# Kernel optimization log

Measured on AMD Instinct MI355X. Metric: run time of the kernel, lower is better.

Reference implementation:

```python
import jax, jax.numpy as jnp
import numpy as np

N = 100000      # nodes
E = 1600000     # edges (avg degree 16)
F_IN = 128
F_OUT = 128
EPS = 1e-5      # BatchNorm eps


def setup_inputs() -> dict:
    key = jax.random.key(0)
    ks = jax.random.split(key, 10)
    s_in = 1.0 / np.sqrt(F_IN)
    s_out = 1.0 / np.sqrt(F_OUT)
    return {
        "x": jax.random.normal(ks[0], (N, F_IN), dtype=jnp.float32),
        "edge_index": jax.random.randint(ks[1], (2, E), 0, N, dtype=jnp.int32),
        # layer 0: SAGEConv(F_IN, F_OUT, aggr='max'); lin_l has bias, lin_r does not
        "W0_l": jax.random.normal(ks[2], (F_IN, F_OUT), dtype=jnp.float32) * s_in,
        "b0_l": jnp.zeros((F_OUT,), dtype=jnp.float32),
        "W0_r": jax.random.normal(ks[3], (F_IN, F_OUT), dtype=jnp.float32) * s_in,
        "gamma0": jnp.ones((F_OUT,), dtype=jnp.float32),
        "beta0": jnp.zeros((F_OUT,), dtype=jnp.float32),
        # layer 1: SAGEConv(F_OUT, F_OUT, aggr='max')
        "W1_l": jax.random.normal(ks[4], (F_OUT, F_OUT), dtype=jnp.float32) * s_out,
        "b1_l": jnp.zeros((F_OUT,), dtype=jnp.float32),
        "W1_r": jax.random.normal(ks[5], (F_OUT, F_OUT), dtype=jnp.float32) * s_out,
        "gamma1": jnp.ones((F_OUT,), dtype=jnp.float32),
        "beta1": jnp.zeros((F_OUT,), dtype=jnp.float32),
    }


def _sage_conv_max(x, src, dst, W_l, b_l, W_r):
    # gather source features along edges, scatter-max into destination nodes
    msgs = x[src]                                             # [E, F]
    agg = jax.ops.segment_max(msgs, dst, num_segments=N)      # [N, F], -inf for isolated
    agg = jnp.where(jnp.isfinite(agg), agg, 0.0)              # PyG fills empty segments with 0
    return agg @ W_l + b_l + x @ W_r                          # lin_l(aggr) + lin_r(x)


def _batch_norm(h, gamma, beta):
    mu = jnp.mean(h, axis=0)
    var = jnp.var(h, axis=0)
    return (h - mu) * jax.lax.rsqrt(var + EPS) * gamma + beta


def reference(x, edge_index, W0_l, b0_l, W0_r, gamma0, beta0,
              W1_l, b1_l, W1_r, gamma1, beta1):
    src, dst = edge_index[0], edge_index[1]
    h = _sage_conv_max(x, src, dst, W0_l, b0_l, W0_r)
    h = jax.nn.relu(_batch_norm(h, gamma0, beta0))
    h = _sage_conv_max(h, src, dst, W1_l, b1_l, W1_r)
    h = jax.nn.relu(_batch_norm(h, gamma1, beta1))
    return h
```

## Files before the change

kernel.cpp:

```cpp
#include <hip/hip_runtime.h>
#include <stdint.h>

#define EPS_BN 1e-5f

typedef __attribute__((ext_vector_type(8))) short short8v;
typedef __attribute__((ext_vector_type(4))) float f32x4;

__device__ __forceinline__ unsigned rne_bf16(float f) {
    unsigned u = __float_as_uint(f);
    return (u + 0x7FFFu + ((u >> 16) & 1u)) >> 16;
}

extern "C" __global__ __launch_bounds__(256)
void f32_to_bf16_kernel(const float4* __restrict__ in, uint2* __restrict__ out, long n4) {
    long i = (long)blockIdx.x * 256 + threadIdx.x;
    long stride = (long)gridDim.x * 256;
    for (; i < n4; i += stride) {
        float4 v = in[i];
        uint2 o;
        o.x = rne_bf16(v.x) | (rne_bf16(v.y) << 16);
        o.y = rne_bf16(v.z) | (rne_bf16(v.w) << 16);
        out[i] = o;
    }
}

extern "C" __global__ __launch_bounds__(256)
void wt_prep_kernel(const float* __restrict__ Wl, const float* __restrict__ Wr,
                    unsigned short* __restrict__ Wt) {
    int idx = blockIdx.x * 256 + threadIdx.x;
    int col = idx >> 8, k = idx & 255;
    float v = (k < 128) ? Wl[(size_t)k * 128 + col] : Wr[(size_t)(k - 128) * 128 + col];
    Wt[(size_t)col * 256 + k] = (unsigned short)rne_bf16(v);
}

extern "C" __global__ __launch_bounds__(256)
void init_head_kernel(int* __restrict__ head, int n) {
    int i = blockIdx.x * 256 + threadIdx.x;
    if (i < n) head[i] = -1;
}

extern "C" __global__ __launch_bounds__(256)
void link_kernel(const int* __restrict__ ei, int* __restrict__ head,
                 uint2* __restrict__ pair, int E) {
    int e = blockIdx.x * 256 + threadIdx.x;
    if (e < E) {
        int src = ei[e];
        int dst = ei[E + e];
        int old = atomicExch(&head[dst], e);
        uint2 p; p.x = (unsigned)src; p.y = (unsigned)old;
        pair[e] = p;
    }
}

extern "C" __global__ __launch_bounds__(256, 8)
void gather_max_ll16_kernel(const uint4* __restrict__ x16r, const int* __restrict__ head,
                            const uint2* __restrict__ pair,
                            uint4* __restrict__ agg16, float* __restrict__ stats, int Nn) {
    if (blockIdx.x == 0 && threadIdx.x < 256) stats[threadIdx.x] = 0.0f;
    int t = blockIdx.x * 256 + threadIdx.x;
    int node = t >> 4;
    if (node >= Nn) return;
    int lane = t & 15;
    int e = head[node];
    uint4 out;
    if (e >= 0) {
        uint2 p = pair[e];
        uint4 r = x16r[(size_t)p.x * 16 + lane];
        float a0 = __uint_as_float(r.x << 16), a1 = __uint_as_float(r.x);
        float a2 = __uint_as_float(r.y << 16), a3 = __uint_as_float(r.y);
        float a4 = __uint_as_float(r.z << 16), a5 = __uint_as_float(r.z);
        float a6 = __uint_as_float(r.w << 16), a7 = __uint_as_float(r.w);
        int en = (int)p.y;
        while (en >= 0) {
            uint2 pn = pair[en];
            uint4 v = x16r[(size_t)pn.x * 16 + lane];
            en = (int)pn.y;
            a0 = fmaxf(a0, __uint_as_float(v.x << 16));
            a1 = fmaxf(a1, __uint_as_float(v.x));
            a2 = fmaxf(a2, __uint_as_float(v.y << 16));
            a3 = fmaxf(a3, __uint_as_float(v.y));
            a4 = fmaxf(a4, __uint_as_float(v.z << 16));
            a5 = fmaxf(a5, __uint_as_float(v.z));
            a6 = fmaxf(a6, __uint_as_float(v.w << 16));
            a7 = fmaxf(a7, __uint_as_float(v.w));
        }
        out.x = (__float_as_uint(a0) >> 16) | (__float_as_uint(a1) & 0xFFFF0000u);
        out.y = (__float_as_uint(a2) >> 16) | (__float_as_uint(a3) & 0xFFFF0000u);
        out.z = (__float_as_uint(a4) >> 16) | (__float_as_uint(a5) & 0xFFFF0000u);
        out.w = (__float_as_uint(a6) >> 16) | (__float_as_uint(a7) & 0xFFFF0000u);
    } else {
        out.x = out.y = out.z = out.w = 0u;
    }
    agg16[(size_t)node * 16 + lane] = out;
}

extern "C" __global__ __launch_bounds__(256)
void gemm_bf16_kernel(const unsigned short* __restrict__ agg16,
                      const unsigned short* __restrict__ xin16,
                      const unsigned short* __restrict__ Wt,
                      const float* __restrict__ bias,
                      float* __restrict__ h, float* __restrict__ stats, int nrows) {
    __shared__ float redS[4][128];
    __shared__ float redQ[4][128];

    const int t = threadIdx.x;
    const int w = t >> 6, l = t & 63;
    const int wm = w >> 1, wn = w & 1;
    const int r16 = l & 15, g = l >> 4;
    const int blockRow = blockIdx.x * 128;
    const int colBase = wn * 64;

    f32x4 acc[4][4];
#pragma unroll
    for (int m = 0; m < 4; ++m)
#pragma unroll
        for (int n = 0; n < 4; ++n) acc[m][n] = (f32x4){0.f, 0.f, 0.f, 0.f};

    const short8v az = {0, 0, 0, 0, 0, 0, 0, 0};

#pragma unroll
    for (int kt = 0; kt < 8; ++kt) {
        const unsigned short* Asrc = (kt < 4) ? agg16 : xin16;
        const int kofs = (kt < 4) ? kt * 32 : kt * 32 - 128;

        short8v b[4];
#pragma unroll
        for (int n = 0; n < 4; ++n) {
            int col = colBase + n * 16 + r16;
            b[n] = *(const short8v*)(Wt + (size_t)col * 256 + kt * 32 + g * 8);
        }
        short8v a[4];
#pragma unroll
        for (int m = 0; m < 4; ++m) {
            int row = blockRow + wm * 64 + m * 16 + r16;
            a[m] = (row < nrows)
                 ? *(const short8v*)(Asrc + (size_t)row * 128 + kofs + g * 8)
                 : az;
        }
#pragma unroll
        for (int m = 0; m < 4; ++m)
#pragma unroll
            for (int n = 0; n < 4; ++n)
                acc[m][n] = __builtin_amdgcn_mfma_f32_16x16x32_bf16(a[m], b[n], acc[m][n], 0, 0, 0);
    }

    for (int i = t; i < 512; i += 256) {
        ((float*)redS)[i] = 0.f;
        ((float*)redQ)[i] = 0.f;
    }
    __syncthreads();

    float bcol[4];
#pragma unroll
    for (int n = 0; n < 4; ++n) bcol[n] = bias[colBase + n * 16 + r16];

    float s4[4] = {0.f, 0.f, 0.f, 0.f};
    float q4[4] = {0.f, 0.f, 0.f, 0.f};
#pragma unroll
    for (int m = 0; m < 4; ++m) {
#pragma unroll
        for (int reg = 0; reg < 4; ++reg) {
            int row = blockRow + wm * 64 + m * 16 + g * 4 + reg;
            if (row < nrows) {
#pragma unroll
                for (int n = 0; n < 4; ++n) {
                    float o = acc[m][n][reg] + bcol[n];
                    h[(size_t)row * 128 + colBase + n * 16 + r16] = o;
                    s4[n] += o;
                    q4[n] += o * o;
                }
            }
        }
    }
#pragma unroll
    for (int n = 0; n < 4; ++n) {
        s4[n] += __shfl_xor(s4[n], 16, 64);
        s4[n] += __shfl_xor(s4[n], 32, 64);
        q4[n] += __shfl_xor(q4[n], 16, 64);
        q4[n] += __shfl_xor(q4[n], 32, 64);
    }
    if (g == 0) {
#pragma unroll
        for (int n = 0; n < 4; ++n) {
            redS[w][colBase + n * 16 + r16] = s4[n];
            redQ[w][colBase + n * 16 + r16] = q4[n];
        }
    }
    __syncthreads();
    if (t < 128) {
        float s = redS[0][t] + redS[1][t] + redS[2][t] + redS[3][t];
        float q = redQ[0][t] + redQ[1][t] + redQ[2][t] + redQ[3][t];
        atomicAdd(&stats[t], s);
        atomicAdd(&stats[128 + t], q);
    }
}

extern "C" __global__
void zero_stats_kernel(float* __restrict__ stats) {
    stats[threadIdx.x] = 0.0f;
}

extern "C" __global__
void finalize_kernel(const float* __restrict__ stats, const float* __restrict__ gamma,
                     const float* __restrict__ beta, float* __restrict__ ss, float inv_n) {
    int c = threadIdx.x;
    if (c < 128) {
        float mu = stats[c] * inv_n;
        float var = stats[128 + c] * inv_n - mu * mu;
        float sc = gamma[c] * rsqrtf(var + EPS_BN);
        ss[c] = sc;
        ss[128 + c] = beta[c] - mu * sc;
    }
}

extern "C" __global__ __launch_bounds__(256)
void bn_relu_tobf16_kernel(const float4* __restrict__ h, const float* __restrict__ ss,
                           uint2* __restrict__ y16, long n4) {
    __shared__ float s_ss[256];
    if (threadIdx.x < 256) s_ss[threadIdx.x] = ss[threadIdx.x];
    __syncthreads();
    long i = (long)blockIdx.x * blockDim.x + threadIdx.x;
    long stride = (long)gridDim.x * blockDim.x;
    for (; i < n4; i += stride) {
        int c4 = (int)(i & 31) * 4;
        float4 v = h[i];
        float o0 = fmaxf(fmaf(v.x, s_ss[c4 + 0], s_ss[128 + c4 + 0]), 0.f);
        float o1 = fmaxf(fmaf(v.y, s_ss[c4 + 1], s_ss[128 + c4 + 1]), 0.f);
        float o2 = fmaxf(fmaf(v.z, s_ss[c4 + 2], s_ss[128 + c4 + 2]), 0.f);
        float o3 = fmaxf(fmaf(v.w, s_ss[c4 + 3], s_ss[128 + c4 + 3]), 0.f);
        uint2 o;
        o.x = rne_bf16(o0) | (rne_bf16(o1) << 16);
        o.y = rne_bf16(o2) | (rne_bf16(o3) << 16);
        y16[i] = o;
    }
}

extern "C" __global__ __launch_bounds__(256)
void bn_relu_kernel(float4* __restrict__ h, const float* __restrict__ ss, long n4) {
    __shared__ float s_ss[256];
    if (threadIdx.x < 256) s_ss[threadIdx.x] = ss[threadIdx.x];
    __syncthreads();
    long i = (long)blockIdx.x * blockDim.x + threadIdx.x;
    long stride = (long)gridDim.x * blockDim.x;
    for (; i < n4; i += stride) {
        int c4 = (int)(i & 31) * 4;
        float4 v = h[i];
        v.x = fmaxf(fmaf(v.x, s_ss[c4 + 0], s_ss[128 + c4 + 0]), 0.f);
        v.y = fmaxf(fmaf(v.y, s_ss[c4 + 1], s_ss[128 + c4 + 1]), 0.f);
        v.z = fmaxf(fmaf(v.z, s_ss[c4 + 2], s_ss[128 + c4 + 2]), 0.f);
        v.w = fmaxf(fmaf(v.w, s_ss[c4 + 3], s_ss[128 + c4 + 3]), 0.f);
        h[i] = v;
    }
}

__device__ __forceinline__ unsigned map_f(float f) {
    unsigned u = __float_as_uint(f);
    return (u & 0x80000000u) ? ~u : (u | 0x80000000u);
}
__device__ __forceinline__ float unmap_f(unsigned m) {
    return (m & 0x80000000u) ? __uint_as_float(m & 0x7FFFFFFFu) : __uint_as_float(~m);
}

extern "C" __global__ __launch_bounds__(256)
void init_sentinel_kernel(uint4* __restrict__ agg, long n4) {
    uint4 z = {0u, 0u, 0u, 0u};
    long i = (long)blockIdx.x * blockDim.x + threadIdx.x;
    long stride = (long)gridDim.x * blockDim.x;
    for (; i < n4; i += stride) agg[i] = z;
}

extern "C" __global__ __launch_bounds__(256)
void scatter_max_kernel(const float4* __restrict__ xin, const int* __restrict__ ei,
                        unsigned* __restrict__ agg, int E) {
    int t = blockIdx.x * 256 + threadIdx.x;
    int e = t >> 5;
    if (e >= E) return;
    int f4 = t & 31;
    int src = ei[e];
    int dst = ei[E + e];
    float4 v = xin[(size_t)src * 32 + f4];
    unsigned* p = agg + (size_t)dst * 128 + (size_t)f4 * 4;
    atomicMax(p + 0, map_f(v.x));
    atomicMax(p + 1, map_f(v.y));
    atomicMax(p + 2, map_f(v.z));
    atomicMax(p + 3, map_f(v.w));
}

extern "C" __global__ __launch_bounds__(256)
void unmap_kernel(unsigned* __restrict__ agg, long n) {
    long i = (long)blockIdx.x * blockDim.x + threadIdx.x;
    long stride = (long)gridDim.x * blockDim.x;
    for (; i < n; i += stride) {
        unsigned u = agg[i];
        agg[i] = __float_as_uint(u ? unmap_f(u) : 0.0f);
    }
}

extern "C" __global__ __launch_bounds__(256)
void gemm_kernel(const float* __restrict__ agg, const float* __restrict__ xin,
                 const float* __restrict__ Wl, const float* __restrict__ Wr,
                 const float* __restrict__ bias, float* __restrict__ h,
                 float* __restrict__ stats, int nrows) {
    __shared__ __align__(16) float As[64][36];
    __shared__ __align__(16) float Bs[32][136];
    __shared__ float redS[4][128];
    __shared__ float redQ[4][128];

    const int t = threadIdx.x;
    const int tx = t & 15;
    const int ty = t >> 4;
    const int tx8 = tx * 8;
    const int ty4 = ty * 4;
    const int blockRow = blockIdx.x * 64;

    float acc[4][8];
#pragma unroll
    for (int j = 0; j < 4; ++j)
#pragma unroll
        for (int c = 0; c < 8; ++c) acc[j][c] = 0.0f;

    for (int kt = 0; kt < 8; ++kt) {
        const int k0 = kt * 32;
        const bool isAgg = (kt < 4);
        const float* W = isAgg ? Wl : Wr;
        const float* Asrc = isAgg ? agg : xin;
        const int kw = isAgg ? k0 : (k0 - 128);

#pragma unroll
        for (int it = 0; it < 4; ++it) {
            int idx = t + it * 256;
            int kr = idx >> 5, cq = idx & 31;
            float4 ww = *(const float4*)&W[(size_t)(kw + kr) * 128 + cq * 4];
            *(float4*)&Bs[kr][cq * 4] = ww;
        }
#pragma unroll
        for (int it = 0; it < 2; ++it) {
            int idx = t + it * 256;
            int r = idx >> 3, kq = idx & 7;
            int row_g = blockRow + r;
            float4 a = {0.f, 0.f, 0.f, 0.f};
            if (row_g < nrows)
                a = *(const float4*)&Asrc[(size_t)row_g * 128 + kw + kq * 4];
            *(float4*)&As[r][kq * 4] = a;
        }
        __syncthreads();

#pragma unroll
        for (int kk = 0; kk < 32; ++kk) {
            float aa[4];
            aa[0] = As[ty4 + 0][kk];
            aa[1] = As[ty4 + 1][kk];
            aa[2] = As[ty4 + 2][kk];
            aa[3] = As[ty4 + 3][kk];
            float4 b0 = *(const float4*)&Bs[kk][tx8];
            float4 b1 = *(const float4*)&Bs[kk][tx8 + 4];
            float bb[8] = {b0.x, b0.y, b0.z, b0.w, b1.x, b1.y, b1.z, b1.w};
#pragma unroll
            for (int j = 0; j < 4; ++j)
#pragma unroll
                for (int c = 0; c < 8; ++c)
                    acc[j][c] = fmaf(aa[j], bb[c], acc[j][c]);
        }
        __syncthreads();
    }

    float bv[8];
#pragma unroll
    for (int c = 0; c < 8; ++c) bv[c] = bias[tx8 + c];

    float s_loc[8], q_loc[8];
#pragma unroll
    for (int c = 0; c < 8; ++c) { s_loc[c] = 0.f; q_loc[c] = 0.f; }

#pragma unroll
    for (int j = 0; j < 4; ++j) {
        int row = blockRow + ty4 + j;
        if (row < nrows) {
            float o[8];
#pragma unroll
            for (int c = 0; c < 8; ++c) {
                o[c] = acc[j][c] + bv[c];
                s_loc[c] += o[c];
                q_loc[c] += o[c] * o[c];
            }
            float4 o0 = {o[0], o[1], o[2], o[3]};
            float4 o1 = {o[4], o[5], o[6], o[7]};
            *(float4*)&h[(size_t)row * 128 + tx8] = o0;
            *(float4*)&h[(size_t)row * 128 + tx8 + 4] = o1;
        }
    }

#pragma unroll
    for (int c = 0; c < 8; ++c) {
        s_loc[c] += __shfl_xor(s_loc[c], 16, 64);
        s_loc[c] += __shfl_xor(s_loc[c], 32, 64);
        q_loc[c] += __shfl_xor(q_loc[c], 16, 64);
        q_loc[c] += __shfl_xor(q_loc[c], 32, 64);
    }
    int wave = t >> 6;
    if ((t & 63) < 16) {
#pragma unroll
        for (int c = 0; c < 8; ++c) {
            redS[wave][tx8 + c] = s_loc[c];
            redQ[wave][tx8 + c] = q_loc[c];
        }
    }
    __syncthreads();
    if (t < 128) {
        float s = redS[0][t] + redS[1][t] + redS[2][t] + redS[3][t];
        float q = redQ[0][t] + redQ[1][t] + redQ[2][t] + redQ[3][t];
        atomicAdd(&stats[t], s);
        atomicAdd(&stats[128 + t], q);
    }
}

static void run_layer_bf16(const unsigned short* in16, const int* head, const uint2* pair,
                           int Nn, const unsigned short* Wt, const float* bl,
                           const float* gamma, const float* beta,
                           unsigned short* agg16, float* stats, float* ss,
                           float* h, hipStream_t stream) {
    gather_max_ll16_kernel<<<(Nn * 16 + 255) / 256, 256, 0, stream>>>(
        (const uint4*)in16, head, pair, (uint4*)agg16, stats, Nn);
    gemm_bf16_kernel<<<(Nn + 127) / 128, 256, 0, stream>>>(agg16, in16, Wt, bl,
                                                           h, stats, Nn);
    finalize_kernel<<<1, 128, 0, stream>>>(stats, gamma, beta, ss, 1.0f / (float)Nn);
}

static void run_layer_atomic(const float* in_feat, const int* ei, int Nn, int Ee,
                             const float* Wl, const float* bl, const float* Wr,
                             const float* gamma, const float* beta,
                             float* agg, float* stats, float* ss,
                             float* out, hipStream_t stream) {
    long aggN = (long)Nn * 128;
    long n4 = aggN / 4;

    zero_stats_kernel<<<1, 256, 0, stream>>>(stats);
    int initBlocks = (int)((n4 + 255) / 256);
    if (initBlocks > 4096) initBlocks = 4096;
    init_sentinel_kernel<<<initBlocks, 256, 0, stream>>>((uint4*)agg, n4);
    int sb = (int)(((long)Ee * 32 + 255) / 256);
    scatter_max_kernel<<<sb, 256, 0, stream>>>((const float4*)in_feat, ei,
                                               (unsigned*)agg, Ee);
    int ub = (int)((aggN + 255) / 256);
    if (ub > 8192) ub = 8192;
    unmap_kernel<<<ub, 256, 0, stream>>>((unsigned*)agg, aggN);
    gemm_kernel<<<(Nn + 63) / 64, 256, 0, stream>>>(agg, in_feat, Wl, Wr, bl,
                                                    out, stats, Nn);
    finalize_kernel<<<1, 128, 0, stream>>>(stats, gamma, beta, ss, 1.0f / (float)Nn);
    int bnBlocks = (int)((n4 + 255) / 256);
    if (bnBlocks > 8192) bnBlocks = 8192;
    bn_relu_kernel<<<bnBlocks, 256, 0, stream>>>((float4*)out, ss, n4);
}

extern "C" void kernel_launch(void* const* d_in, const int* in_sizes, int n_in,
                              void* d_out, int out_size, void* d_ws, size_t ws_size,
                              hipStream_t stream) {
    (void)n_in; (void)out_size;
    const float* x     = (const float*)d_in[0];
    const int*   ei    = (const int*)d_in[1];
    const float* W0_l  = (const float*)d_in[2];
    const float* b0_l  = (const float*)d_in[3];
    const float* W0_r  = (const float*)d_in[4];
    const float* g0    = (const float*)d_in[5];
    const float* be0   = (const float*)d_in[6];
    const float* W1_l  = (const float*)d_in[7];
    const float* b1_l  = (const float*)d_in[8];
    const float* W1_r  = (const float*)d_in[9];
    const float* g1    = (const float*)d_in[10];
    const float* be1   = (const float*)d_in[11];

    int Nn = in_sizes[0] / 128;
    int Ee = in_sizes[1] / 2;
    long n4 = (long)Nn * 32;

    char* p = (char*)d_ws;
    unsigned short* xy16 = (unsigned short*)p;  p += (size_t)Nn * 128 * 2;
    unsigned short* agg16 = (unsigned short*)p; p += (size_t)Nn * 128 * 2;
    float* stats = (float*)p;                   p += 256 * sizeof(float);
    float* ss = (float*)p;                      p += 256 * sizeof(float);
    unsigned short* Wt0 = (unsigned short*)p;   p += 128 * 256 * 2;
    unsigned short* Wt1 = (unsigned short*)p;   p += 128 * 256 * 2;
    int* head = (int*)p;                        p += (size_t)Nn * sizeof(int);
    uint2* pair = (uint2*)p;                    p += (size_t)Ee * sizeof(uint2);
    size_t needed = (size_t)(p - (char*)d_ws);
    float* out = (float*)d_out;

    if (ws_size >= needed) {
        int cvB = (int)((n4 + 255) / 256);
        if (cvB > 4096) cvB = 4096;
        f32_to_bf16_kernel<<<cvB, 256, 0, stream>>>((const float4*)x, (uint2*)xy16, n4);
        wt_prep_kernel<<<128, 256, 0, stream>>>(W0_l, W0_r, Wt0);
        wt_prep_kernel<<<128, 256, 0, stream>>>(W1_l, W1_r, Wt1);
        init_head_kernel<<<(Nn + 255) / 256, 256, 0, stream>>>(head, Nn);
        link_kernel<<<(Ee + 255) / 256, 256, 0, stream>>>(ei, head, pair, Ee);

        run_layer_bf16(xy16, head, pair, Nn, Wt0, b0_l, g0, be0,
                       agg16, stats, ss, out, stream);
        int bnB = (int)((n4 + 255) / 256);
        if (bnB > 8192) bnB = 8192;
        bn_relu_tobf16_kernel<<<bnB, 256, 0, stream>>>((const float4*)out, ss,
                                                       (uint2*)xy16, n4);
        run_layer_bf16(xy16, head, pair, Nn, Wt1, b1_l, g1, be1,
                       agg16, stats, ss, out, stream);
        bn_relu_kernel<<<bnB, 256, 0, stream>>>((float4*)out, ss, n4);
    } else {
        float* agg = (float*)d_ws;
        float* fstats = (float*)((char*)d_ws + (size_t)Nn * 128 * sizeof(float));
        float* fss = fstats + 256;
        run_layer_atomic(x, ei, Nn, Ee, W0_l, b0_l, W0_r, g0, be0,
                         agg, fstats, fss, out, stream);
        run_layer_atomic(out, ei, Nn, Ee, W1_l, b1_l, W1_r, g1, be1,
                         agg, fstats, fss, out, stream);
    }
}
```

Baseline: 405.8 us.

## Split per-node edge lists into four chains and fold BN finalize into apply kernels

Each destination node now gets four linked-list heads, picked by the edge id mod 4. The gather kernel walks all four chains together, so four independent pointer-chasing loads can be in flight per step instead of one serial chain, and atomic contention on the head slots is also reduced. Separately, the BN scale/shift finalize kernel is folded into each bn_relu kernel, where every block recomputes it from stats, and the two weight-prep launches are merged into one. This cuts several tiny launches but grows the head array fourfold and adds divergence when the chains differ in length.

```diff
diff --git a/kernel.cpp b/kernel.cpp
--- a/kernel.cpp
+++ b/kernel.cpp
@@ -25,9 +25,15 @@
 }
 
 extern "C" __global__ __launch_bounds__(256)
-void wt_prep_kernel(const float* __restrict__ Wl, const float* __restrict__ Wr,
-                    unsigned short* __restrict__ Wt) {
-    int idx = blockIdx.x * 256 + threadIdx.x;
+void wt_prep2_kernel(const float* __restrict__ Wl0, const float* __restrict__ Wr0,
+                     unsigned short* __restrict__ Wt0,
+                     const float* __restrict__ Wl1, const float* __restrict__ Wr1,
+                     unsigned short* __restrict__ Wt1) {
+    int b = blockIdx.x;
+    const float* Wl = (b < 128) ? Wl0 : Wl1;
+    const float* Wr = (b < 128) ? Wr0 : Wr1;
+    unsigned short* Wt = (b < 128) ? Wt0 : Wt1;
+    int idx = (b & 127) * 256 + threadIdx.x;
     int col = idx >> 8, k = idx & 255;
     float v = (k < 128) ? Wl[(size_t)k * 128 + col] : Wr[(size_t)(k - 128) * 128 + col];
     Wt[(size_t)col * 256 + k] = (unsigned short)rne_bf16(v);
@@ -40,20 +46,30 @@
 }
 
 extern "C" __global__ __launch_bounds__(256)
-void link_kernel(const int* __restrict__ ei, int* __restrict__ head,
+void link_kernel(const int* __restrict__ ei, int* __restrict__ head4,
                  uint2* __restrict__ pair, int E) {
     int e = blockIdx.x * 256 + threadIdx.x;
     if (e < E) {
         int src = ei[e];
         int dst = ei[E + e];
-        int old = atomicExch(&head[dst], e);
+        int old = atomicExch(&head4[dst * 4 + (e & 3)], e);
         uint2 p; p.x = (unsigned)src; p.y = (unsigned)old;
         pair[e] = p;
     }
 }
 
+#define FM8(v)                                              \
+    a0 = fmaxf(a0, __uint_as_float((v).x << 16));           \
+    a1 = fmaxf(a1, __uint_as_float((v).x));                 \
+    a2 = fmaxf(a2, __uint_as_float((v).y << 16));           \
+    a3 = fmaxf(a3, __uint_as_float((v).y));                 \
+    a4 = fmaxf(a4, __uint_as_float((v).z << 16));           \
+    a5 = fmaxf(a5, __uint_as_float((v).z));                 \
+    a6 = fmaxf(a6, __uint_as_float((v).w << 16));           \
+    a7 = fmaxf(a7, __uint_as_float((v).w));
+
 extern "C" __global__ __launch_bounds__(256, 8)
-void gather_max_ll16_kernel(const uint4* __restrict__ x16r, const int* __restrict__ head,
+void gather_max_ll16_kernel(const uint4* __restrict__ x16r, const int* __restrict__ head4,
                             const uint2* __restrict__ pair,
                             uint4* __restrict__ agg16, float* __restrict__ stats, int Nn) {
     if (blockIdx.x == 0 && threadIdx.x < 256) stats[threadIdx.x] = 0.0f;
@@ -61,35 +77,37 @@
     int node = t >> 4;
     if (node >= Nn) return;
     int lane = t & 15;
-    int e = head[node];
+
+    int4 hh = *(const int4*)(head4 + (size_t)node * 4);
+    int e0 = hh.x, e1 = hh.y, e2 = hh.z, e3 = hh.w;
+
     uint4 out;
-    if (e >= 0) {
-        uint2 p = pair[e];
-        uint4 r = x16r[(size_t)p.x * 16 + lane];
-        float a0 = __uint_as_float(r.x << 16), a1 = __uint_as_float(r.x);
-        float a2 = __uint_as_float(r.y << 16), a3 = __uint_as_float(r.y);
-        float a4 = __uint_as_float(r.z << 16), a5 = __uint_as_float(r.z);
-        float a6 = __uint_as_float(r.w << 16), a7 = __uint_as_float(r.w);
-        int en = (int)p.y;
-        while (en >= 0) {
-            uint2 pn = pair[en];
-            uint4 v = x16r[(size_t)pn.x * 16 + lane];
-            en = (int)pn.y;
-            a0 = fmaxf(a0, __uint_as_float(v.x << 16));
-            a1 = fmaxf(a1, __uint_as_float(v.x));
-            a2 = fmaxf(a2, __uint_as_float(v.y << 16));
-            a3 = fmaxf(a3, __uint_as_float(v.y));
-            a4 = fmaxf(a4, __uint_as_float(v.z << 16));
-            a5 = fmaxf(a5, __uint_as_float(v.z));
-            a6 = fmaxf(a6, __uint_as_float(v.w << 16));
-            a7 = fmaxf(a7, __uint_as_float(v.w));
+    if ((e0 & e1 & e2 & e3) < 0 && e0 < 0 && e1 < 0 && e2 < 0 && e3 < 0) {
+        out.x = out.y = out.z = out.w = 0u;
+    } else {
+        float a0 = -INFINITY, a1 = -INFINITY, a2 = -INFINITY, a3 = -INFINITY;
+        float a4 = -INFINITY, a5 = -INFINITY, a6 = -INFINITY, a7 = -INFINITY;
+        while ((e0 & e1 & e2 & e3) >= 0 || e0 >= 0 || e1 >= 0 || e2 >= 0 || e3 >= 0) {
+            bool b0 = e0 >= 0, b1 = e1 >= 0, b2 = e2 >= 0, b3 = e3 >= 0;
+            uint2 p0, p1, p2, p3;
+            uint4 v0, v1, v2, v3;
+            if (b0) p0 = pair[e0];
+            if (b1) p1 = pair[e1];
+            if (b2) p2 = pair[e2];
+            if (b3) p3 = pair[e3];
+            if (b0) v0 = x16r[(size_t)p0.x * 16 + lane];
+            if (b1) v1 = x16r[(size_t)p1.x * 16 + lane];
+            if (b2) v2 = x16r[(size_t)p2.x * 16 + lane];
+            if (b3) v3 = x16r[(size_t)p3.x * 16 + lane];
+            if (b0) { e0 = (int)p0.y; FM8(v0); }
+            if (b1) { e1 = (int)p1.y; FM8(v1); }
+            if (b2) { e2 = (int)p2.y; FM8(v2); }
+            if (b3) { e3 = (int)p3.y; FM8(v3); }
         }
         out.x = (__float_as_uint(a0) >> 16) | (__float_as_uint(a1) & 0xFFFF0000u);
         out.y = (__float_as_uint(a2) >> 16) | (__float_as_uint(a3) & 0xFFFF0000u);
         out.z = (__float_as_uint(a4) >> 16) | (__float_as_uint(a5) & 0xFFFF0000u);
         out.w = (__float_as_uint(a6) >> 16) | (__float_as_uint(a7) & 0xFFFF0000u);
-    } else {
-        out.x = out.y = out.z = out.w = 0u;
     }
     agg16[(size_t)node * 16 + lane] = out;
 }
@@ -195,30 +213,27 @@
     }
 }
 
-extern "C" __global__
-void zero_stats_kernel(float* __restrict__ stats) {
-    stats[threadIdx.x] = 0.0f;
-}
-
-extern "C" __global__
-void finalize_kernel(const float* __restrict__ stats, const float* __restrict__ gamma,
-                     const float* __restrict__ beta, float* __restrict__ ss, float inv_n) {
-    int c = threadIdx.x;
-    if (c < 128) {
-        float mu = stats[c] * inv_n;
-        float var = stats[128 + c] * inv_n - mu * mu;
-        float sc = gamma[c] * rsqrtf(var + EPS_BN);
-        ss[c] = sc;
-        ss[128 + c] = beta[c] - mu * sc;
-    }
-}
-
-extern "C" __global__ __launch_bounds__(256)
-void bn_relu_tobf16_kernel(const float4* __restrict__ h, const float* __restrict__ ss,
-                           uint2* __restrict__ y16, long n4) {
+__device__ __forceinline__ void bn_make_ss(const float* __restrict__ stats,
+                                           const float* __restrict__ gamma,
+                                           const float* __restrict__ beta,
+                                           float inv_n, float* s_ss) {
+    int t = threadIdx.x;
+    if (t < 128) {
+        float mu = stats[t] * inv_n;
+        float var = stats[128 + t] * inv_n - mu * mu;
+        float sc = gamma[t] * rsqrtf(var + EPS_BN);
+        s_ss[t] = sc;
+        s_ss[128 + t] = beta[t] - mu * sc;
+    }
+    __syncthreads();
+}
+
+extern "C" __global__ __launch_bounds__(256)
+void bn_relu_tobf16_kernel(const float4* __restrict__ h, const float* __restrict__ stats,
+                           const float* __restrict__ gamma, const float* __restrict__ beta,
+                           float inv_n, uint2* __restrict__ y16, long n4) {
     __shared__ float s_ss[256];
-    if (threadIdx.x < 256) s_ss[threadIdx.x] = ss[threadIdx.x];
-    __syncthreads();
+    bn_make_ss(stats, gamma, beta, inv_n, s_ss);
     long i = (long)blockIdx.x * blockDim.x + threadIdx.x;
     long stride = (long)gridDim.x * blockDim.x;
     for (; i < n4; i += stride) {
@@ -236,10 +251,11 @@
 }
 
 extern "C" __global__ __launch_bounds__(256)
-void bn_relu_kernel(float4* __restrict__ h, const float* __restrict__ ss, long n4) {
+void bn_relu_f32_kernel(float4* __restrict__ h, const float* __restrict__ stats,
+                        const float* __restrict__ gamma, const float* __restrict__ beta,
+                        float inv_n, long n4) {
     __shared__ float s_ss[256];
-    if (threadIdx.x < 256) s_ss[threadIdx.x] = ss[threadIdx.x];
-    __syncthreads();
+    bn_make_ss(stats, gamma, beta, inv_n, s_ss);
     long i = (long)blockIdx.x * blockDim.x + threadIdx.x;
     long stride = (long)gridDim.x * blockDim.x;
     for (; i < n4; i += stride) {
@@ -296,6 +312,11 @@
     }
 }
 
+extern "C" __global__
+void zero_stats_kernel(float* __restrict__ stats) {
+    stats[threadIdx.x] = 0.0f;
+}
+
 extern "C" __global__ __launch_bounds__(256)
 void gemm_kernel(const float* __restrict__ agg, const float* __restrict__ xin,
                  const float* __restrict__ Wl, const float* __restrict__ Wr,
@@ -414,23 +435,10 @@
     }
 }
 
-static void run_layer_bf16(const unsigned short* in16, const int* head, const uint2* pair,
-                           int Nn, const unsigned short* Wt, const float* bl,
-                           const float* gamma, const float* beta,
-                           unsigned short* agg16, float* stats, float* ss,
-                           float* h, hipStream_t stream) {
-    gather_max_ll16_kernel<<<(Nn * 16 + 255) / 256, 256, 0, stream>>>(
-        (const uint4*)in16, head, pair, (uint4*)agg16, stats, Nn);
-    gemm_bf16_kernel<<<(Nn + 127) / 128, 256, 0, stream>>>(agg16, in16, Wt, bl,
-                                                           h, stats, Nn);
-    finalize_kernel<<<1, 128, 0, stream>>>(stats, gamma, beta, ss, 1.0f / (float)Nn);
-}
-
 static void run_layer_atomic(const float* in_feat, const int* ei, int Nn, int Ee,
                              const float* Wl, const float* bl, const float* Wr,
                              const float* gamma, const float* beta,
-                             float* agg, float* stats, float* ss,
-                             float* out, hipStream_t stream) {
+                             float* agg, float* stats, float* out, hipStream_t stream) {
     long aggN = (long)Nn * 128;
     long n4 = aggN / 4;
 
@@ -446,10 +454,10 @@
     unmap_kernel<<<ub, 256, 0, stream>>>((unsigned*)agg, aggN);
     gemm_kernel<<<(Nn + 63) / 64, 256, 0, stream>>>(agg, in_feat, Wl, Wr, bl,
                                                     out, stats, Nn);
-    finalize_kernel<<<1, 128, 0, stream>>>(stats, gamma, beta, ss, 1.0f / (float)Nn);
     int bnBlocks = (int)((n4 + 255) / 256);
     if (bnBlocks > 8192) bnBlocks = 8192;
-    bn_relu_kernel<<<bnBlocks, 256, 0, stream>>>((float4*)out, ss, n4);
+    bn_relu_f32_kernel<<<bnBlocks, 256, 0, stream>>>((float4*)out, stats, gamma, beta,
+                                                     1.0f / (float)Nn, n4);
 }
 
 extern "C" void kernel_launch(void* const* d_in, const int* in_sizes, int n_in,
@@ -472,15 +480,15 @@
     int Nn = in_sizes[0] / 128;
     int Ee = in_sizes[1] / 2;
     long n4 = (long)Nn * 32;
+    float inv_n = 1.0f / (float)Nn;
 
     char* p = (char*)d_ws;
     unsigned short* xy16 = (unsigned short*)p;  p += (size_t)Nn * 128 * 2;
     unsigned short* agg16 = (unsigned short*)p; p += (size_t)Nn * 128 * 2;
     float* stats = (float*)p;                   p += 256 * sizeof(float);
-    float* ss = (float*)p;                      p += 256 * sizeof(float);
     unsigned short* Wt0 = (unsigned short*)p;   p += 128 * 256 * 2;
     unsigned short* Wt1 = (unsigned short*)p;   p += 128 * 256 * 2;
-    int* head = (int*)p;                        p += (size_t)Nn * sizeof(int);
+    int* head4 = (int*)p;                       p += (size_t)Nn * 4 * sizeof(int);
     uint2* pair = (uint2*)p;                    p += (size_t)Ee * sizeof(uint2);
     size_t needed = (size_t)(p - (char*)d_ws);
     float* out = (float*)d_out;
@@ -489,27 +497,31 @@
         int cvB = (int)((n4 + 255) / 256);
         if (cvB > 4096) cvB = 4096;
         f32_to_bf16_kernel<<<cvB, 256, 0, stream>>>((const float4*)x, (uint2*)xy16, n4);
-        wt_prep_kernel<<<128, 256, 0, stream>>>(W0_l, W0_r, Wt0);
-        wt_prep_kernel<<<128, 256, 0, stream>>>(W1_l, W1_r, Wt1);
-        init_head_kernel<<<(Nn + 255) / 256, 256, 0, stream>>>(head, Nn);
-        link_kernel<<<(Ee + 255) / 256, 256, 0, stream>>>(ei, head, pair, Ee);
-
-        run_layer_bf16(xy16, head, pair, Nn, Wt0, b0_l, g0, be0,
-                       agg16, stats, ss, out, stream);
+        wt_prep2_kernel<<<256, 256, 0, stream>>>(W0_l, W0_r, Wt0, W1_l, W1_r, Wt1);
+        init_head_kernel<<<(Nn * 4 + 255) / 256, 256, 0, stream>>>(head4, Nn * 4);
+        link_kernel<<<(Ee + 255) / 256, 256, 0, stream>>>(ei, head4, pair, Ee);
+
         int bnB = (int)((n4 + 255) / 256);
         if (bnB > 8192) bnB = 8192;
-        bn_relu_tobf16_kernel<<<bnB, 256, 0, stream>>>((const float4*)out, ss,
-                                                       (uint2*)xy16, n4);
-        run_layer_bf16(xy16, head, pair, Nn, Wt1, b1_l, g1, be1,
-                       agg16, stats, ss, out, stream);
-        bn_relu_kernel<<<bnB, 256, 0, stream>>>((float4*)out, ss, n4);
+
+        gather_max_ll16_kernel<<<(Nn * 16 + 255) / 256, 256, 0, stream>>>(
+            (const uint4*)xy16, head4, pair, (uint4*)agg16, stats, Nn);
+        gemm_bf16_kernel<<<(Nn + 127) / 128, 256, 0, stream>>>(agg16, xy16, Wt0, b0_l,
+                                                               out, stats, Nn);
+        bn_relu_tobf16_kernel<<<bnB, 256, 0, stream>>>((const float4*)out, stats, g0, be0,
+                                                       inv_n, (uint2*)xy16, n4);
+        gather_max_ll16_kernel<<<(Nn * 16 + 255) / 256, 256, 0, stream>>>(
+            (const uint4*)xy16, head4, pair, (uint4*)agg16, stats, Nn);
+        gemm_bf16_kernel<<<(Nn + 127) / 128, 256, 0, stream>>>(agg16, xy16, Wt1, b1_l,
+                                                               out, stats, Nn);
+        bn_relu_f32_kernel<<<bnB, 256, 0, stream>>>((float4*)out, stats, g1, be1,
+                                                    inv_n, n4);
     } else {
         float* agg = (float*)d_ws;
         float* fstats = (float*)((char*)d_ws + (size_t)Nn * 128 * sizeof(float));
-        float* fss = fstats + 256;
         run_layer_atomic(x, ei, Nn, Ee, W0_l, b0_l, W0_r, g0, be0,
-                         agg, fstats, fss, out, stream);
+                         agg, fstats, out, stream);
         run_layer_atomic(out, ei, Nn, Ee, W1_l, b1_l, W1_r, g1, be1,
-                         agg, fstats, fss, out, stream);
-    }
-}
+                         agg, fstats, out, stream);
+    }
+}
```

After: 419.9 us. +3.5%, slower.
